# Kernel tuning notes

Hardware: AMD Instinct MI355X
Metric: run time of the kernel (lower is better)

The kernel has to match this reference:

```python
import jax, jax.numpy as jnp
import numpy as np

B, L, D = 4, 2048, 1024
H, DH = 16, 64
W = 128            # window_len
CS, R = 32, 1      # chunk_size, chunk_rank
CACHE = 2048
NCC = CACHE // CS * R   # compressed cache vectors (64)
NCB = L // CS * R       # compressed block vectors (64)
NC = NCC + NCB          # total compressed vectors (128)
NQ = L // CS            # query chunks (64)
T = L // W              # query tiles (16)
NEG = jnp.float32(-1e30)


def _ln(x, g, b, eps=1e-5):
    m = x.mean(-1, keepdims=True)
    v = ((x - m) ** 2).mean(-1, keepdims=True)
    return (x - m) * jax.lax.rsqrt(v + eps) * g + b


def _scores(x, Wd, bd):
    # dconv_1 + per-chunk softmax over chunk_size positions
    b = x.shape[0]; nc = x.shape[1] // CS
    s = (x @ Wd + bd).reshape(b, nc, CS, H, R)
    s = jnp.transpose(s, (0, 3, 1, 4, 2))          # b,H,nc,R,CS
    return jax.nn.softmax(s.astype(jnp.float32), axis=-1).astype(x.dtype)


def _compress(x, sc):
    b = x.shape[0]; nc = x.shape[1] // CS
    xv = jnp.transpose(x.reshape(b, nc, CS, H, DH), (0, 3, 1, 2, 4))  # b,H,nc,CS,DH
    return (sc @ xv).reshape(b, H, nc * R, DH)


def _heads(x):
    b, l, _ = x.shape
    return jnp.transpose(x.reshape(b, l, H, DH), (0, 2, 1, 3))


def _rel_shift(x):
    # Transformer-XL style relative shift, chunk variant (zeros enter from padding)
    b = x.shape[0]; nc = x.shape[-1]
    x5 = jnp.transpose(x.reshape(b, H, NQ, CS, nc), (0, 1, 3, 2, 4))  # b,H,CS,NQ,nc
    xp = jnp.pad(x5, ((0, 0), (0, 0), (0, 0), (0, 0), (0, R))).reshape(b, H, CS, NQ * (nc + R))
    idx = NQ * R + jnp.arange(NQ)[:, None] * nc + jnp.arange(nc)[None, :]
    out = jnp.take(xp, idx.reshape(-1), axis=-1).reshape(b, H, CS, NQ, nc)
    return jnp.transpose(out, (0, 1, 3, 2, 4)).reshape(b, H, L, nc)


def _forward(h, h_cache, key_pe, pos_win, Wq, Wk, Wv, Wo, Wd, bd, Wr, br, Wrc, brc,
             r_r_bias, r_w_bias, g_dproj, b_dproj, g_win, b_win, mask):
    b = h.shape[0]
    q = _heads(h @ Wq) / np.float32(np.sqrt(DH))       # b,H,L,DH (pre-scaled)

    # --- compressed cache keys/values ---
    hcc = _compress(h_cache, _scores(h_cache, Wd, bd))           # b,H,NCC,DH
    hcm = jnp.transpose(hcc, (0, 2, 1, 3)).reshape(b, -1, D)
    k_cache = _heads(_ln(hcm @ Wk, g_dproj, b_dproj))
    v_cache = _heads(_ln(hcm @ Wv, g_dproj, b_dproj))

    # --- sliding window keys/values (last W of cache + current block) ---
    k_bp = h @ Wk
    v_bp = h @ Wv
    hw = h_cache[:, -W:]
    k_win = _ln(jnp.concatenate([hw @ Wk, k_bp], 1), g_win, b_win)   # b, W+L, D
    v_win = _ln(jnp.concatenate([hw @ Wv, v_bp], 1), g_win, b_win)

    # --- compressed current-block keys/values ---
    sc = _scores(h, Wd, bd)
    k_bpc = _heads(_ln(jnp.transpose(_compress(k_bp, sc), (0, 2, 1, 3)).reshape(b, -1, D), g_dproj, b_dproj))
    v_bpc = _heads(_ln(jnp.transpose(_compress(v_bp, sc), (0, 2, 1, 3)).reshape(b, -1, D), g_dproj, b_dproj))
    k_comp = jnp.concatenate([k_cache, k_bpc], 2)     # b,H,NC,DH
    v_comp = jnp.concatenate([v_cache, v_bpc], 2)

    # --- windowed attention (tiled, as_strided equivalent via gather) ---
    ti = jnp.arange(T)[:, None] * W + jnp.arange(2 * W)[None, :]     # (T, 2W)
    k_t = jnp.transpose(k_win[:, ti].reshape(b, T, 2 * W, H, DH), (0, 3, 1, 2, 4))  # b,H,T,2W,DH
    v_t = jnp.transpose(v_win[:, ti].reshape(b, T, 2 * W, H, DH), (0, 3, 1, 2, 4))
    q_t = q.reshape(b, H, T, W, DH)
    aw = jnp.einsum('bhtqd,bhtkd->bhtqk', q_t + r_w_bias, k_t)       # b,H,T,W,2W
    # diagonal extraction: row q keeps cols q+1 .. q+W (the W causal window keys)
    dcol = jnp.arange(W)[:, None] + 1 + jnp.arange(W)[None, :]       # (W, W)
    aw = jnp.take_along_axis(aw, dcol[None, None, None], axis=-1).reshape(b, H, L, W)
    pos_t = (pos_win @ Wr + br).reshape(W, H, DH)
    aw = aw + jnp.einsum('bhld,whd->bhlw', q + r_r_bias, pos_t)

    # --- compressed (chunk) attention ---
    ac = jnp.einsum('bhld,bhcd->bhlc', q, k_comp)
    pos_c = (key_pe @ Wrc + brc).reshape(NC, H, DH)
    ac = ac + _rel_shift(jnp.einsum('bhld,chd->bhlc', q, pos_c))
    ac = jnp.where(mask, NEG, ac.reshape(b, H, NQ, CS, NC)).reshape(b, H, L, NC)

    # --- joint softmax over [compressed | window] ---
    full = jax.nn.softmax(jnp.concatenate([ac, aw], -1).astype(jnp.float32), -1).astype(h.dtype)
    ac, aw = full[..., :NC], full[..., NC:]

    # --- put_tiles: scatter window probs back to tiled 2W layout (inverse of diag extract) ---
    awt = aw.reshape(b, H, T, W, W)
    awp = jnp.pad(awt, ((0, 0), (0, 0), (0, 0), (0, 0), (1, W)))     # last dim 1+2W, zeros outside band
    col = jnp.clip(jnp.arange(2 * W)[None, :] - jnp.arange(W)[:, None], 0, 2 * W)
    aw_t = jnp.take_along_axis(awp, col[None, None, None], axis=-1)  # b,H,T,W,2W

    out = jnp.einsum('bhlc,bhcd->bhld', ac, v_comp) + \
          jnp.einsum('bhtqk,bhtkd->bhtqd', aw_t, v_t).reshape(b, H, L, DH)
    out = jnp.transpose(out, (0, 2, 1, 3)).reshape(b, L, D)
    return out @ Wo


def setup_inputs() -> dict:
    key = jax.random.key(0)
    ks = jax.random.split(key, 16)
    p = lambda i, shape: jax.random.normal(ks[i], shape, jnp.float32) * 0.02
    inp = dict(
        h=jax.random.normal(ks[0], (B, L, D), jnp.float32),
        h_cache=jax.random.normal(ks[1], (B, CACHE, D), jnp.float32),
        key_pe=jax.random.normal(ks[2], (NC, D), jnp.float32),
        pos_embed_window=jax.random.normal(ks[3], (W, D), jnp.float32),
        Wq=p(4, (D, D)), Wk=p(5, (D, D)), Wv=p(6, (D, D)), Wo=p(7, (D, D)),
        Wd=p(8, (D, H * R)), bd=jnp.zeros((H * R,), jnp.float32),
        Wr=p(9, (D, D)), br=jnp.zeros((D,), jnp.float32),
        Wrc=p(10, (D, D)), brc=jnp.zeros((D,), jnp.float32),
        r_r_bias=p(11, (1, H, 1, DH)), r_w_bias=p(12, (1, H, 1, 1, DH)),
        g_dproj=jnp.ones((D,), jnp.float32), b_dproj=jnp.zeros((D,), jnp.float32),
        g_win=jnp.ones((D,), jnp.float32), b_win=jnp.zeros((D,), jnp.float32),
    )
    # causal mask over compressed vectors: bp chunk c visible to query chunk j only if c < j
    jq = jnp.arange(NQ)[:, None]
    cc = jnp.arange(NCB // R)[None, :]
    mbp = jnp.repeat(cc >= jq, R, axis=1)                         # (NQ, NCB)
    mask = jnp.concatenate([jnp.zeros((NQ, NCC), bool), mbp], axis=1)
    inp['chunked_attn_mask'] = mask[None, None, :, None, :]       # (1,1,NQ,1,NC)
    return inp


def reference(h, h_cache, key_pe, pos_embed_window, Wq, Wk, Wv, Wo, Wd, bd, Wr, br,
              Wrc, brc, r_r_bias, r_w_bias, g_dproj, b_dproj, g_win, b_win,
              chunked_attn_mask):
    return _forward(h, h_cache, key_pe, pos_embed_window, Wq, Wk, Wv, Wo, Wd, bd,
                    Wr, br, Wrc, brc, r_r_bias, r_w_bias, g_dproj, b_dproj,
                    g_win, b_win, chunked_attn_mask)
```

## Files before the change

kernel.cpp:

```cpp
#include <hip/hip_runtime.h>


typedef unsigned short u16;
typedef __attribute__((ext_vector_type(8))) short short8;
typedef __attribute__((ext_vector_type(4))) float f32x4;

#define NEGINF -1e30f

__device__ __forceinline__ float bf2f(u16 u) {
    union { unsigned int i; float f; } v; v.i = ((unsigned int)u) << 16; return v.f;
}
__device__ __forceinline__ u16 f2bf(float f) {
    union { float fl; unsigned int i; } v; v.fl = f;
    unsigned int x = v.i;
    return (u16)((x + 0x7fffu + ((x >> 16) & 1u)) >> 16);
}
__device__ __forceinline__ short8 ldg8(const u16* p) { return *(const short8*)p; }

__device__ __forceinline__ void async16(const u16* g, u16* l) {
    __builtin_amdgcn_global_load_lds(
        (const __attribute__((address_space(1))) unsigned int*)g,
        (__attribute__((address_space(3))) unsigned int*)l, 16, 0, 0);
}

__global__ __launch_bounds__(256) void cast_all(
    const float* __restrict__ h, const float* __restrict__ hc,
    const float* __restrict__ pos_w, const float* __restrict__ key_pe,
    const float* __restrict__ Wd,
    u16* __restrict__ hB, u16* __restrict__ hcwB,
    u16* __restrict__ pwB, u16* __restrict__ kpeB, u16* __restrict__ WdB)
{
    const int bx = blockIdx.x, tid = threadIdx.x;
    if (bx < 8192) {
        int i = bx * 256 + tid;
        float4 v = ((const float4*)h)[i];
        u16* o = hB + (long)i * 4;
        o[0] = f2bf(v.x); o[1] = f2bf(v.y); o[2] = f2bf(v.z); o[3] = f2bf(v.w);
    } else if (bx < 8704) {
        int i = (bx - 8192) * 256 + tid;
        int flat = i * 4;
        int b = flat >> 17, r = (flat >> 10) & 127, c = flat & 1023;
        float4 v = *(const float4*)(hc + ((long)b * 2048 + 1920 + r) * 1024 + c);
        u16* o = hcwB + (long)flat;
        o[0] = f2bf(v.x); o[1] = f2bf(v.y); o[2] = f2bf(v.z); o[3] = f2bf(v.w);
    } else if (bx < 8832) {
        int i = (bx - 8704) * 256 + tid;
        float4 v = ((const float4*)pos_w)[i];
        u16* o = pwB + (long)i * 4;
        o[0] = f2bf(v.x); o[1] = f2bf(v.y); o[2] = f2bf(v.z); o[3] = f2bf(v.w);
    } else if (bx < 8960) {
        int i = (bx - 8832) * 256 + tid;
        float4 v = ((const float4*)key_pe)[i];
        u16* o = kpeB + (long)i * 4;
        o[0] = f2bf(v.x); o[1] = f2bf(v.y); o[2] = f2bf(v.z); o[3] = f2bf(v.w);
    } else {
        int e = (bx - 8960) * 256 + tid;
        if (e < 16384) WdB[(e & 15) * 1024 + (e >> 4)] = f2bf(Wd[e]);
    }
}

__global__ __launch_bounds__(256) void cast_transpose6(
    const float* __restrict__ W0, const float* __restrict__ W1,
    const float* __restrict__ W2, const float* __restrict__ W3,
    const float* __restrict__ W4, const float* __restrict__ W5,
    u16* __restrict__ D0, u16* __restrict__ D1, u16* __restrict__ D2,
    u16* __restrict__ D3, u16* __restrict__ D4, u16* __restrict__ D5)
{
    const int z = blockIdx.z;
    const float* W = (z == 0) ? W0 : (z == 1) ? W1 : (z == 2) ? W2
                   : (z == 3) ? W3 : (z == 4) ? W4 : W5;
    u16* WT = (z == 0) ? D0 : (z == 1) ? D1 : (z == 2) ? D2
            : (z == 3) ? D3 : (z == 4) ? D4 : D5;

    __shared__ float t[32][33];
    const int bx = blockIdx.x, by = blockIdx.y;
    const int tx = threadIdx.x & 31, ty = threadIdx.x >> 5;
    #pragma unroll
    for (int p = 0; p < 4; ++p) {
        int k = by * 32 + ty + p * 8;
        t[ty + p * 8][tx] = W[(long)k * 1024 + bx * 32 + tx];
    }
    __syncthreads();
    #pragma unroll
    for (int p = 0; p < 4; ++p) {
        int n = ty + p * 8;
        WT[((long)(bx * 32 + n)) * 1024 + by * 32 + tx] = f2bf(t[tx][n]);
    }
}

__global__ __launch_bounds__(512) void gemm_qkv_big(
    const u16* __restrict__ A, const u16* __restrict__ Bt,
    u16* __restrict__ q_ws, u16* __restrict__ kbp, u16* __restrict__ vbp)
{
    const int tid = threadIdx.x;
    const int bm = blockIdx.x, bn = blockIdx.y;
    const int K = 1024, NT = 32;

    __shared__ __align__(16) u16 smem[65536 / 2];
    u16* const As = smem;
    u16* const Bs = smem + 16384;

    const int lane = tid & 63, wv = tid >> 6;
    const int l15 = lane & 15, quad = lane >> 4;
    const int wm = (wv >> 2) * 128, wn = (wv & 3) * 64;

    f32x4 acc[8][4];
    #pragma unroll
    for (int i = 0; i < 8; ++i)
        #pragma unroll
        for (int j = 0; j < 4; ++j) acc[i][j] = (f32x4){0.f, 0.f, 0.f, 0.f};

    const int r_in = lane >> 2, col8 = (lane & 3) * 8;
    const bool isA = (wv < 4);
    const int crow0 = (isA ? wv : wv - 4) * 64;
    const u16* gb = isA ? (A + (long)(bm * 256 + crow0 + r_in) * K)
                        : (Bt + (long)(bn * 256 + crow0 + r_in) * K);
    const u16* s0 = gb + col8;
    const u16* s1 = s0 + (long)16 * K;
    const u16* s2 = s0 + (long)32 * K;
    const u16* s3 = s0 + (long)48 * K;
    u16* const lb = (isA ? As : Bs) + crow0 * 32;

    auto stage = [&](int buf) {
        u16* d = lb + buf * 8192;
        async16(s0, d);
        async16(s1, d + 512);
        async16(s2, d + 1024);
        async16(s3, d + 1536);
        s0 += 32; s1 += 32; s2 += 32; s3 += 32;
    };

    stage(0);
    for (int t = 0; t < NT; ++t) {
        __builtin_amdgcn_s_barrier();
        if (t + 1 < NT) {
            stage((t + 1) & 1);
            asm volatile("s_waitcnt vmcnt(4) lgkmcnt(0)\ns_barrier" ::: "memory");
        } else {
            asm volatile("s_waitcnt vmcnt(0) lgkmcnt(0)\ns_barrier" ::: "memory");
        }
        const u16* as = As + (t & 1) * 8192;
        const u16* bs = Bs + (t & 1) * 8192;
        short8 af[8], bfr[4];
        #pragma unroll
        for (int i = 0; i < 8; ++i)
            af[i] = *(const short8*)&as[(wm + i * 16 + l15) * 32 + quad * 8];
        #pragma unroll
        for (int j = 0; j < 4; ++j)
            bfr[j] = *(const short8*)&bs[(wn + j * 16 + l15) * 32 + quad * 8];
        #pragma unroll
        for (int i = 0; i < 8; ++i)
            #pragma unroll
            for (int j = 0; j < 4; ++j)
                acc[i][j] = __builtin_amdgcn_mfma_f32_16x16x32_bf16(af[i], bfr[j], acc[i][j], 0, 0, 0);
    }

    const int mat = bn >> 2;
    u16* const outp = (mat == 0) ? q_ws : (mat == 1) ? kbp : vbp;
    const float scl = (mat == 0) ? 0.125f : 1.f;
    const int colbase = (bn & 3) * 256;
    #pragma unroll
    for (int hh = 0; hh < 2; ++hh) {
        __syncthreads();
        if ((wv >> 2) == hh) {
            #pragma unroll
            for (int i = 0; i < 8; ++i) {
                #pragma unroll
                for (int j = 0; j < 4; ++j) {
                    const int row = i * 16 + quad * 4;
                    const int col = wn + j * 16 + l15;
                    smem[(row + 0) * 256 + col] = f2bf(acc[i][j][0] * scl);
                    smem[(row + 1) * 256 + col] = f2bf(acc[i][j][1] * scl);
                    smem[(row + 2) * 256 + col] = f2bf(acc[i][j][2] * scl);
                    smem[(row + 3) * 256 + col] = f2bf(acc[i][j][3] * scl);
                }
            }
        }
        __syncthreads();
        #pragma unroll
        for (int k = 0; k < 8; ++k) {
            const int seg = tid + k * 512;
            const int row = seg >> 5, c16 = seg & 31;
            short8 v = *(const short8*)&smem[row * 256 + c16 * 8];
            *(short8*)(outp + (long)(bm * 256 + hh * 128 + row) * 1024 + colbase + c16 * 8) = v;
        }
    }
}

#define GEMM_P3_BODY(EPILOGUE)                                                  \
    const int tid = threadIdx.x;                                                \
    const int bm = blockIdx.x, bn = blockIdx.y;                                 \
    const int K = 1024, NT = 32;                                                \
    __shared__ __align__(16) u16 As[3 * 128 * 32];                              \
    __shared__ __align__(16) u16 Bs[3 * 128 * 32];                              \
    const int lane = tid & 63, wv = tid >> 6;                                   \
    const int l15 = lane & 15, quad = lane >> 4;                                \
    const int wm = (wv & 1) * 64, wn = (wv >> 1) * 64;                          \
    f32x4 acc[4][4];                                                            \
    _Pragma("unroll")                                                           \
    for (int i = 0; i < 4; ++i)                                                 \
        _Pragma("unroll")                                                       \
        for (int j = 0; j < 4; ++j) acc[i][j] = (f32x4){0.f, 0.f, 0.f, 0.f};    \
    const int srow = wv * 32 + (lane >> 2);                                     \
    const int scol = (lane & 3) * 8;                                            \
    const u16* a_src  = A  + (long)(bm * 128 + srow) * K + scol;                \
    const u16* a_src2 = a_src + (long)16 * K;                                   \
    const u16* b_src  = Bt + (long)(bn * 128 + srow) * K + scol;                \
    const u16* b_src2 = b_src + (long)16 * K;                                   \
    const int lofs0 = (wv * 32) * 32;                                           \
    const int lofs1 = (wv * 32 + 16) * 32;                                      \
    auto stage = [&](int t, int cur) {                                          \
        const int k0 = t * 32;                                                  \
        async16(a_src  + k0, &As[cur * 4096 + lofs0]);                          \
        async16(a_src2 + k0, &As[cur * 4096 + lofs1]);                          \
        async16(b_src  + k0, &Bs[cur * 4096 + lofs0]);                          \
        async16(b_src2 + k0, &Bs[cur * 4096 + lofs1]);                          \
    };                                                                          \
    stage(0, 0); stage(1, 1);                                                   \
    int cur = 0;                                                                \
    for (int t = 0; t < NT; ++t) {                                              \
        if (t == NT - 1)                                                        \
            asm volatile("s_waitcnt vmcnt(0) lgkmcnt(0)\ns_barrier" ::: "memory"); \
        else                                                                    \
            asm volatile("s_waitcnt vmcnt(4) lgkmcnt(0)\ns_barrier" ::: "memory"); \
        int nxt = cur + 2; if (nxt >= 3) nxt -= 3;                              \
        if (t + 2 < NT) stage(t + 2, nxt);                                      \
        const u16* as = &As[cur * 4096];                                        \
        const u16* bs = &Bs[cur * 4096];                                        \
        short8 af[4], bfr[4];                                                   \
        _Pragma("unroll")                                                       \
        for (int i = 0; i < 4; ++i)                                             \
            af[i] = *(const short8*)&as[(wm + i * 16 + l15) * 32 + quad * 8];   \
        _Pragma("unroll")                                                       \
        for (int j = 0; j < 4; ++j)                                             \
            bfr[j] = *(const short8*)&bs[(wn + j * 16 + l15) * 32 + quad * 8];  \
        _Pragma("unroll")                                                       \
        for (int i = 0; i < 4; ++i)                                             \
            _Pragma("unroll")                                                   \
            for (int j = 0; j < 4; ++j)                                         \
                acc[i][j] = __builtin_amdgcn_mfma_f32_16x16x32_bf16(af[i], bfr[j], acc[i][j], 0, 0, 0); \
        cur = (cur + 1 == 3) ? 0 : cur + 1;                                     \
    }                                                                           \
    EPILOGUE

__global__ __launch_bounds__(256) void gemm_out3(
    const u16* __restrict__ A, const u16* __restrict__ Bt,
    float* __restrict__ Cf)
{
    GEMM_P3_BODY({
        _Pragma("unroll")
        for (int i = 0; i < 4; ++i) {
            _Pragma("unroll")
            for (int j = 0; j < 4; ++j) {
                int col = bn * 128 + wn + j * 16 + l15;
                _Pragma("unroll")
                for (int r = 0; r < 4; ++r) {
                    int row = bm * 128 + wm + i * 16 + quad * 4 + r;
                    Cf[(long)row * 1024 + col] = acc[i][j][r];
                }
            }
        }
    })
}

struct GJob {
    const u16* A; long ab;
    const u16* Bt;
    float* Cf; u16* Cb; long cb;
    const float* bias; float scale;
};

__device__ __forceinline__ void gemm_core128(
    const GJob& j, int bz, int bm, int bn, int N, int K)
{
    const int tid = threadIdx.x;
    const u16* A = j.A + (long)bz * j.ab;
    const long coff = (long)bz * j.cb;

    __shared__ __align__(16) u16 As[128 * 32];
    __shared__ __align__(16) u16 Bs[128 * 32];

    const int lane = tid & 63, wv = tid >> 6;
    const int l15 = lane & 15, quad = lane >> 4;
    const int wm = (wv & 1) * 64, wn = (wv >> 1) * 64;

    f32x4 acc[4][4];
    #pragma unroll
    for (int i = 0; i < 4; ++i)
        #pragma unroll
        for (int jx = 0; jx < 4; ++jx) acc[i][jx] = (f32x4){0.f, 0.f, 0.f, 0.f};

    const int srow = wv * 32 + (lane >> 2);
    const int scol = (lane & 3) * 8;
    const u16* a_src  = A    + (long)(bm * 128 + srow) * K + scol;
    const u16* a_src2 = a_src + (long)16 * K;
    const u16* b_src  = j.Bt + (long)(bn * 128 + srow) * K + scol;
    const u16* b_src2 = b_src + (long)16 * K;
    u16* lA0 = &As[(wv * 32) * 32];
    u16* lA1 = &As[(wv * 32 + 16) * 32];
    u16* lB0 = &Bs[(wv * 32) * 32];
    u16* lB1 = &Bs[(wv * 32 + 16) * 32];

    for (int k0 = 0; k0 < K; k0 += 32) {
        async16(a_src, lA0); async16(a_src2, lA1);
        async16(b_src, lB0); async16(b_src2, lB1);
        a_src += 32; a_src2 += 32; b_src += 32; b_src2 += 32;
        __syncthreads();
        short8 af[4], bfr[4];
        #pragma unroll
        for (int i = 0; i < 4; ++i)
            af[i] = *(const short8*)&As[(wm + i * 16 + l15) * 32 + quad * 8];
        #pragma unroll
        for (int jx = 0; jx < 4; ++jx)
            bfr[jx] = *(const short8*)&Bs[(wn + jx * 16 + l15) * 32 + quad * 8];
        #pragma unroll
        for (int i = 0; i < 4; ++i)
            #pragma unroll
            for (int jx = 0; jx < 4; ++jx)
                acc[i][jx] = __builtin_amdgcn_mfma_f32_16x16x32_bf16(af[i], bfr[jx], acc[i][jx], 0, 0, 0);
        __syncthreads();
    }

    #pragma unroll
    for (int i = 0; i < 4; ++i) {
        #pragma unroll
        for (int jx = 0; jx < 4; ++jx) {
            int col = bn * 128 + wn + jx * 16 + l15;
            float bsv = j.bias ? j.bias[col] : 0.f;
            #pragma unroll
            for (int r = 0; r < 4; ++r) {
                int row = bm * 128 + wm + i * 16 + quad * 4 + r;
                float v = acc[i][jx][r] * j.scale + bsv;
                long idx = coff + (long)row * N + col;
                if (j.Cf) j.Cf[idx] = v;
                if (j.Cb) j.Cb[idx] = f2bf(v);
            }
        }
    }
}

__global__ __launch_bounds__(256) void gemm_dual(GJob j0, GJob j1, int nz0, int N, int K)
{
    const bool first = ((int)blockIdx.z < nz0);
    const int bz = first ? blockIdx.z : blockIdx.z - nz0;
    if (first) gemm_core128(j0, bz, blockIdx.x, blockIdx.y, N, K);
    else       gemm_core128(j1, bz, blockIdx.x, blockIdx.y, N, K);
}

__global__ __launch_bounds__(256) void gemm_multi4(GJob j0, GJob j1, GJob j2, GJob j3,
                                                   int n0, int n1, int n2, int N, int K)
{
    const int z = blockIdx.z;
    if (z < n0)                gemm_core128(j0, z, blockIdx.x, blockIdx.y, N, K);
    else if (z < n0 + n1)      gemm_core128(j1, z - n0, blockIdx.x, blockIdx.y, N, K);
    else if (z < n0 + n1 + n2) gemm_core128(j2, z - n0 - n1, blockIdx.x, blockIdx.y, N, K);
    else                       gemm_core128(j3, z - n0 - n1 - n2, blockIdx.x, blockIdx.y, N, K);
}

__global__ __launch_bounds__(256) void scores_compress2(
    const float* __restrict__ hc, const u16* __restrict__ hBp,
    const u16* __restrict__ WdB, const float* __restrict__ bd,
    u16* __restrict__ hcm, float* __restrict__ sc_blk)
{
    const int c = blockIdx.x, b = blockIdx.y;
    const bool zc = (blockIdx.z == 0);
    const int tid = threadIdx.x;
    const int lane = tid & 63, wv = tid >> 6;
    const int l15 = lane & 15, quad = lane >> 4;

    __shared__ __align__(16) u16 srcs[32][1032];
    __shared__ float sred[4][32][16];
    __shared__ float s_sm[32][16];

    if (zc) {
        const float* sb = hc + (long)b * 2048 * 1024 + (long)c * 32 * 1024;
        for (int e = tid; e < 8192; e += 256) {
            int flat = e * 4;
            int row = flat >> 10, col = flat & 1023;
            float4 v = *(const float4*)(sb + (long)row * 1024 + col);
            u16* dp = &srcs[row][col];
            dp[0] = f2bf(v.x); dp[1] = f2bf(v.y); dp[2] = f2bf(v.z); dp[3] = f2bf(v.w);
        }
    } else {
        const u16* sb = hBp + (long)b * 2048 * 1024 + (long)c * 32 * 1024;
        for (int e = tid; e < 4096; e += 256) {
            int flat = e * 8;
            int row = flat >> 10, col = flat & 1023;
            *(short8*)&srcs[row][col] = ldg8(sb + (long)row * 1024 + col);
        }
    }
    __syncthreads();

    {
        f32x4 acc0 = {0.f,0.f,0.f,0.f}, acc1 = {0.f,0.f,0.f,0.f};
        const int kq = wv * 256;
        #pragma unroll
        for (int kc = 0; kc < 8; ++kc) {
            int off = kq + kc * 32 + quad * 8;
            short8 bf_ = ldg8(WdB + (long)l15 * 1024 + off);
            short8 a0 = *(const short8*)&srcs[l15][off];
            short8 a1 = *(const short8*)&srcs[16 + l15][off];
            acc0 = __builtin_amdgcn_mfma_f32_16x16x32_bf16(a0, bf_, acc0, 0, 0, 0);
            acc1 = __builtin_amdgcn_mfma_f32_16x16x32_bf16(a1, bf_, acc1, 0, 0, 0);
        }
        #pragma unroll
        for (int r = 0; r < 4; ++r) {
            sred[wv][quad * 4 + r][l15]      = acc0[r];
            sred[wv][16 + quad * 4 + r][l15] = acc1[r];
        }
    }
    __syncthreads();
    for (int idx = tid; idx < 512; idx += 256) {
        int i = idx >> 4, hd = idx & 15;
        s_sm[i][hd] = bd[hd] + sred[0][i][hd] + sred[1][i][hd]
                            + sred[2][i][hd] + sred[3][i][hd];
    }
    __syncthreads();

    if (tid < 16) {
        int hd = tid;
        float m = NEGINF;
        for (int i = 0; i < 32; ++i) m = fmaxf(m, s_sm[i][hd]);
        float s = 0.f;
        for (int i = 0; i < 32; ++i) s += __expf(s_sm[i][hd] - m);
        float inv = 1.f / s;
        for (int i = 0; i < 32; ++i) s_sm[i][hd] = __expf(s_sm[i][hd] - m) * inv;
    }
    __syncthreads();

    if (!zc) {
        for (int idx = tid; idx < 512; idx += 256) {
            int hd = idx >> 5, i = idx & 31;
            sc_blk[(long)b * (16*64*32) + ((long)hd * 64 + c) * 32 + i] = s_sm[i][hd];
        }
    } else {
        #pragma unroll
        for (int p = 0; p < 4; ++p) {
            int j = tid + p * 256;
            int hd = j >> 6;
            float acc = 0.f;
            for (int i = 0; i < 32; ++i) acc += s_sm[i][hd] * bf2f(srcs[i][j]);
            hcm[(long)b * (64*1024) + (long)c * 1024 + j] = f2bf(acc);
        }
    }
}

__global__ __launch_bounds__(256) void compress_kv_ln(
    const u16* __restrict__ kbp, const u16* __restrict__ vbp,
    const float* __restrict__ sc,
    const float* __restrict__ g, const float* __restrict__ be,
    u16* __restrict__ k_comp, u16* __restrict__ vcT)
{
    const int c = blockIdx.x, b = blockIdx.y;
    const int tid = threadIdx.x;
    const int lane = tid & 63, wv = tid >> 6;

    __shared__ float scw[16][32];
    __shared__ float red[4][4];

    for (int idx = tid; idx < 512; idx += 256) {
        int hd = idx >> 5, i = idx & 31;
        scw[hd][i] = sc[((long)(b * 16 + hd) * 64 + c) * 32 + i];
    }
    __syncthreads();

    const int j0 = tid * 4;
    const int hd = j0 >> 6;
    float xk[4] = {0.f,0.f,0.f,0.f}, xv[4] = {0.f,0.f,0.f,0.f};
    const u16* kb = kbp + ((long)b * 2048 + c * 32) * 1024 + j0;
    const u16* vb = vbp + ((long)b * 2048 + c * 32) * 1024 + j0;
    for (int i = 0; i < 32; ++i) {
        float w = scw[hd][i];
        uint2 kr = *(const uint2*)(kb + (long)i * 1024);
        uint2 vr = *(const uint2*)(vb + (long)i * 1024);
        const u16* kp = (const u16*)&kr;
        const u16* vp = (const u16*)&vr;
        #pragma unroll
        for (int p = 0; p < 4; ++p) {
            xk[p] += w * bf2f(kp[p]);
            xv[p] += w * bf2f(vp[p]);
        }
    }
    float sk = 0.f, qk = 0.f, sv = 0.f, qv = 0.f;
    #pragma unroll
    for (int p = 0; p < 4; ++p) { sk += xk[p]; qk += xk[p]*xk[p]; sv += xv[p]; qv += xv[p]*xv[p]; }
    for (int off = 32; off; off >>= 1) {
        sk += __shfl_xor(sk, off); qk += __shfl_xor(qk, off);
        sv += __shfl_xor(sv, off); qv += __shfl_xor(qv, off);
    }
    if (lane == 0) { red[0][wv] = sk; red[1][wv] = qk; red[2][wv] = sv; red[3][wv] = qv; }
    __syncthreads();
    sk = red[0][0] + red[0][1] + red[0][2] + red[0][3];
    qk = red[1][0] + red[1][1] + red[1][2] + red[1][3];
    sv = red[2][0] + red[2][1] + red[2][2] + red[2][3];
    qv = red[3][0] + red[3][1] + red[3][2] + red[3][3];
    const float inv_n = 1.f / 1024.f;
    float mk = sk * inv_n, mv = sv * inv_n;
    float ik = rsqrtf(fmaxf(qk * inv_n - mk * mk, 0.f) + 1e-5f);
    float iv = rsqrtf(fmaxf(qv * inv_n - mv * mv, 0.f) + 1e-5f);
    float4 g4 = *(const float4*)(g + j0);
    float4 b4 = *(const float4*)(be + j0);
    float gg[4] = {g4.x, g4.y, g4.z, g4.w};
    float bb[4] = {b4.x, b4.y, b4.z, b4.w};
    u16 ko[4];
    #pragma unroll
    for (int p = 0; p < 4; ++p) ko[p] = f2bf((xk[p] - mk) * ik * gg[p] + bb[p]);
    *(uint2*)&k_comp[((long)b * 128 + 64 + c) * 1024 + j0] = *(const uint2*)ko;
    #pragma unroll
    for (int p = 0; p < 4; ++p)
        vcT[((long)b * 1024 + j0 + p) * 128 + 64 + c] = f2bf((xv[p] - mv) * iv * gg[p] + bb[p]);
}

__global__ __launch_bounds__(256) void ln_rows_kv(
    const float* __restrict__ kc, const float* __restrict__ vc,
    const float* __restrict__ g, const float* __restrict__ be,
    u16* __restrict__ k_comp, u16* __restrict__ vcT)
{
    const int gr = blockIdx.x;
    const int b = gr >> 6, r = gr & 63;
    const float* pk = kc + ((long)b * 64 + r) * 1024;
    const float* pv = vc + ((long)b * 64 + r) * 1024;
    const int tid = threadIdx.x;
    const int lane = tid & 63, wv = tid >> 6;

    __shared__ float red[4][4];
    float xk[4], xv[4];
    float smk = 0.f, sqk = 0.f, smv = 0.f, sqv = 0.f;
    #pragma unroll
    for (int p = 0; p < 4; ++p) {
        xk[p] = pk[tid + p * 256];
        xv[p] = pv[tid + p * 256];
        smk += xk[p]; sqk += xk[p] * xk[p];
        smv += xv[p]; sqv += xv[p] * xv[p];
    }
    for (int off = 32; off; off >>= 1) {
        smk += __shfl_xor(smk, off); sqk += __shfl_xor(sqk, off);
        smv += __shfl_xor(smv, off); sqv += __shfl_xor(sqv, off);
    }
    if (lane == 0) { red[0][wv] = smk; red[1][wv] = sqk; red[2][wv] = smv; red[3][wv] = sqv; }
    __syncthreads();
    smk = red[0][0] + red[0][1] + red[0][2] + red[0][3];
    sqk = red[1][0] + red[1][1] + red[1][2] + red[1][3];
    smv = red[2][0] + red[2][1] + red[2][2] + red[2][3];
    sqv = red[3][0] + red[3][1] + red[3][2] + red[3][3];
    const float inv_n = 1.f / 1024.f;
    float mk = smk * inv_n, mv = smv * inv_n;
    float ik = rsqrtf(fmaxf(sqk * inv_n - mk * mk, 0.f) + 1e-5f);
    float iv = rsqrtf(fmaxf(sqv * inv_n - mv * mv, 0.f) + 1e-5f);
    #pragma unroll
    for (int p = 0; p < 4; ++p) {
        int j = tid + p * 256;
        k_comp[((long)b * 128 + r) * 1024 + j] = f2bf((xk[p] - mk) * ik * g[j] + be[j]);
        vcT[((long)b * 1024 + j) * 128 + r]    = f2bf((xv[p] - mv) * iv * g[j] + be[j]);
    }
}

__global__ __launch_bounds__(256) void row_stats_all(
    const float* __restrict__ kcw, const float* __restrict__ vcw,
    const u16* __restrict__ kbp, const u16* __restrict__ vbp,
    float2* __restrict__ st_k, float2* __restrict__ st_v)
{
    const int gr = blockIdx.x;
    const int tid = threadIdx.x;
    const int lane = tid & 63, wv = tid >> 6;

    float sm1 = 0.f, sq1 = 0.f, sm2 = 0.f, sq2 = 0.f;
    long dst;
    if (gr < 512) {
        const int b = gr >> 7, r = gr & 127;
        const float* p1 = kcw + ((long)b * 128 + r) * 1024;
        const float* p2 = vcw + ((long)b * 128 + r) * 1024;
        #pragma unroll
        for (int p = 0; p < 4; ++p) {
            float x = p1[tid + p * 256];
            float y = p2[tid + p * 256];
            sm1 += x; sq1 += x * x;
            sm2 += y; sq2 += y * y;
        }
        dst = (long)b * 2176 + r;
    } else {
        const int g2 = gr - 512;
        const int b = g2 >> 11, r = g2 & 2047;
        const u16* p1 = kbp + ((long)b * 2048 + r) * 1024 + tid * 4;
        const u16* p2 = vbp + ((long)b * 2048 + r) * 1024 + tid * 4;
        uint2 v1 = *(const uint2*)p1;
        uint2 v2 = *(const uint2*)p2;
        const u16* a1 = (const u16*)&v1;
        const u16* a2 = (const u16*)&v2;
        #pragma unroll
        for (int p = 0; p < 4; ++p) {
            float x = bf2f(a1[p]);
            float y = bf2f(a2[p]);
            sm1 += x; sq1 += x * x;
            sm2 += y; sq2 += y * y;
        }
        dst = (long)b * 2176 + 128 + r;
    }

    __shared__ float red[4][4];
    for (int off = 32; off; off >>= 1) {
        sm1 += __shfl_xor(sm1, off); sq1 += __shfl_xor(sq1, off);
        sm2 += __shfl_xor(sm2, off); sq2 += __shfl_xor(sq2, off);
    }
    if (lane == 0) { red[0][wv] = sm1; red[1][wv] = sq1; red[2][wv] = sm2; red[3][wv] = sq2; }
    __syncthreads();
    if (tid == 0) {
        sm1 = red[0][0] + red[0][1] + red[0][2] + red[0][3];
        sq1 = red[1][0] + red[1][1] + red[1][2] + red[1][3];
        sm2 = red[2][0] + red[2][1] + red[2][2] + red[2][3];
        sq2 = red[3][0] + red[3][1] + red[3][2] + red[3][3];
        float m1 = sm1 * (1.f / 1024.f);
        float i1 = rsqrtf(fmaxf(sq1 * (1.f / 1024.f) - m1 * m1, 0.f) + 1e-5f);
        float m2 = sm2 * (1.f / 1024.f);
        float i2 = rsqrtf(fmaxf(sq2 * (1.f / 1024.f) - m2 * m2, 0.f) + 1e-5f);
        st_k[dst] = make_float2(m1, i1);
        st_v[dst] = make_float2(m2, i2);
    }
}

__global__ __launch_bounds__(256) void win_apply(
    const float* __restrict__ kcw, const float* __restrict__ vcw,
    const u16* __restrict__ kbp, const u16* __restrict__ vbp,
    const float2* __restrict__ st_kw, const float2* __restrict__ st_vw,
    const float* __restrict__ g_w, const float* __restrict__ b_w,
    u16* __restrict__ kwin, u16* __restrict__ vwinT)
{
    const int tt = blockIdx.x, dc = blockIdx.y, b = blockIdx.z;
    const int t0 = tt * 64, d0 = dc * 64;
    const int tid = threadIdx.x;

    __shared__ u16 vt[64][74];

    const int r = tid >> 2;
    const int dsub = (tid & 3) * 16;
    const int t = t0 + r;
    float2 sk = st_kw[(long)b * 2176 + t];
    float2 sv = st_vw[(long)b * 2176 + t];
    const float* ksf = kcw + ((long)b * 128 + t) * 1024;
    const float* vsf = vcw + ((long)b * 128 + t) * 1024;
    const u16*   ksb = kbp + ((long)b * 2048 + t - 128) * 1024;
    const u16*   vsb = vbp + ((long)b * 2048 + t - 128) * 1024;
    #pragma unroll
    for (int j = 0; j < 16; j += 4) {
        int d = d0 + dsub + j;
        float4 kv, vv;
        if (t < 128) {
            kv = *(const float4*)(ksf + d);
            vv = *(const float4*)(vsf + d);
        } else {
            uint2 kr = *(const uint2*)(ksb + d);
            uint2 vr = *(const uint2*)(vsb + d);
            const u16* kp = (const u16*)&kr;
            const u16* vp = (const u16*)&vr;
            kv = make_float4(bf2f(kp[0]), bf2f(kp[1]), bf2f(kp[2]), bf2f(kp[3]));
            vv = make_float4(bf2f(vp[0]), bf2f(vp[1]), bf2f(vp[2]), bf2f(vp[3]));
        }
        float4 g4 = *(const float4*)(g_w + d);
        float4 b4 = *(const float4*)(b_w + d);
        u16 ko[4];
        ko[0] = f2bf((kv.x - sk.x) * sk.y * g4.x + b4.x);
        ko[1] = f2bf((kv.y - sk.x) * sk.y * g4.y + b4.y);
        ko[2] = f2bf((kv.z - sk.x) * sk.y * g4.z + b4.z);
        ko[3] = f2bf((kv.w - sk.x) * sk.y * g4.w + b4.w);
        *(uint2*)&kwin[((long)b * 2176 + t) * 1024 + d] = *(const uint2*)ko;
        vt[r][dsub + j + 0] = f2bf((vv.x - sv.x) * sv.y * g4.x + b4.x);
        vt[r][dsub + j + 1] = f2bf((vv.y - sv.x) * sv.y * g4.y + b4.y);
        vt[r][dsub + j + 2] = f2bf((vv.z - sv.x) * sv.y * g4.z + b4.z);
        vt[r][dsub + j + 3] = f2bf((vv.w - sv.x) * sv.y * g4.w + b4.w);
    }
    __syncthreads();
    #pragma unroll
    for (int pass = 0; pass < 16; ++pass) {
        int dd = (tid >> 6) + pass * 4;
        int rr = tid & 63;
        int crow = t0 + rr;
        if (crow >= 1)
            vwinT[((long)b * 1024 + d0 + dd) * 2176 + crow - 1] = vt[rr][dd];
    }
}

__global__ __launch_bounds__(256, 4) void attention(
    const u16* __restrict__ qb,
    const u16* __restrict__ kcb,
    const u16* __restrict__ vcT,
    const u16* __restrict__ kwb,
    const u16* __restrict__ vwT,
    const u16* __restrict__ pcb,
    const u16* __restrict__ ptb,
    const float* __restrict__ r_w,
    const float* __restrict__ r_r,
    u16* __restrict__ attn_o)
{
    const int qc = blockIdx.x, h = blockIdx.y, b = blockIdx.z;
    const int l0 = qc * 32;
    const int tid = threadIdx.x;
    const int lane = tid & 63, wv = tid >> 6;
    const int l15 = lane & 15, quad = lane >> 4;

    __shared__ __align__(16) float L[32 * 260];
    __shared__ __align__(16) u16 qa[32][72];
    u16* Lu = (u16*)L;

    {
        const int r = tid >> 3, d0 = (tid & 7) * 8;
        short8 qv = ldg8(qb + ((long)(b * 2048 + l0 + r)) * 1024 + h * 64 + d0);
        *(short8*)&qa[r][d0] = qv;
    }
    __syncthreads();

    __builtin_amdgcn_s_setprio(1);
    #pragma unroll
    for (int ti = 0; ti < 2; ++ti) {
        int n0 = (wv * 2 + ti) * 16;
        int ci = n0 + l15;
        f32x4 a0 = {0.f,0.f,0.f,0.f}, a1 = {0.f,0.f,0.f,0.f};
        if (n0 < 64 + qc) {
            int p = 64 + ci - qc; if (p > 127) p = 127;
            #pragma unroll
            for (int kc = 0; kc < 2; ++kc) {
                int k0 = kc * 32;
                short8 bk = ldg8(kcb + ((long)(b * 128 + ci)) * 1024 + h * 64 + k0 + quad * 8);
                short8 bp = ldg8(pcb + (long)p * 1024 + h * 64 + k0 + quad * 8);
                short8 fa0 = *(const short8*)&qa[l15][k0 + quad * 8];
                short8 fa1 = *(const short8*)&qa[16 + l15][k0 + quad * 8];
                a0 = __builtin_amdgcn_mfma_f32_16x16x32_bf16(fa0, bk, a0, 0, 0, 0);
                a0 = __builtin_amdgcn_mfma_f32_16x16x32_bf16(fa0, bp, a0, 0, 0, 0);
                a1 = __builtin_amdgcn_mfma_f32_16x16x32_bf16(fa1, bk, a1, 0, 0, 0);
                a1 = __builtin_amdgcn_mfma_f32_16x16x32_bf16(fa1, bp, a1, 0, 0, 0);
            }
        }
        bool msk = (ci >= 64 + qc);
        #pragma unroll
        for (int r = 0; r < 4; ++r) {
            L[(quad * 4 + r) * 260 + ci]      = msk ? NEGINF : a0[r];
            L[(16 + quad * 4 + r) * 260 + ci] = msk ? NEGINF : a1[r];
        }
    }

    {
        short8 qf[2][2];
        #pragma unroll
        for (int kc = 0; kc < 2; ++kc) {
            const int off = kc * 32 + quad * 8;
            const float* bp_ = r_r + h * 64 + off;
            float4 b0 = *(const float4*)bp_;
            float4 b1 = *(const float4*)(bp_ + 4);
            float bb[8] = {b0.x,b0.y,b0.z,b0.w,b1.x,b1.y,b1.z,b1.w};
            #pragma unroll
            for (int hf = 0; hf < 2; ++hf) {
                short8 qv = *(const short8*)&qa[hf * 16 + l15][off];
                short8 f;
                #pragma unroll
                for (int j = 0; j < 8; ++j) f[j] = (short)f2bf(bf2f((u16)qv[j]) + bb[j]);
                qf[kc][hf] = f;
            }
        }
        #pragma unroll
        for (int ti = 0; ti < 2; ++ti) {
            int w0 = (wv * 2 + ti) * 16;
            int w = w0 + l15;
            f32x4 a0 = {0.f,0.f,0.f,0.f}, a1 = {0.f,0.f,0.f,0.f};
            #pragma unroll
            for (int kc = 0; kc < 2; ++kc) {
                int k0 = kc * 32;
                short8 bp = ldg8(ptb + (long)w * 1024 + h * 64 + k0 + quad * 8);
                a0 = __builtin_amdgcn_mfma_f32_16x16x32_bf16(qf[kc][0], bp, a0, 0, 0, 0);
                a1 = __builtin_amdgcn_mfma_f32_16x16x32_bf16(qf[kc][1], bp, a1, 0, 0, 0);
            }
            #pragma unroll
            for (int r = 0; r < 4; ++r) {
                L[(quad * 4 + r) * 260 + 128 + w]      = a0[r];
                L[(16 + quad * 4 + r) * 260 + 128 + w] = a1[r];
            }
        }
    }

    f32x4 s1a[3], s1b[3];
    int nts[3]; int nw = 0;
    {
        short8 qf[2][2];
        #pragma unroll
        for (int kc = 0; kc < 2; ++kc) {
            const int off = kc * 32 + quad * 8;
            const float* bp_ = r_w + h * 64 + off;
            float4 b0 = *(const float4*)bp_;
            float4 b1 = *(const float4*)(bp_ + 4);
            float bb[8] = {b0.x,b0.y,b0.z,b0.w,b1.x,b1.y,b1.z,b1.w};
            #pragma unroll
            for (int hf = 0; hf < 2; ++hf) {
                short8 qv = *(const short8*)&qa[hf * 16 + l15][off];
                short8 f;
                #pragma unroll
                for (int j = 0; j < 8; ++j) f[j] = (short)f2bf(bf2f((u16)qv[j]) + bb[j]);
                qf[kc][hf] = f;
            }
        }
        for (int nt = wv; nt < 10; nt += 4) {
            int t = nt * 16 + l15;
            int row = l0 + 1 + t; if (row > 2175) row = 2175;
            f32x4 a0 = {0.f,0.f,0.f,0.f}, a1 = {0.f,0.f,0.f,0.f};
            #pragma unroll
            for (int kc = 0; kc < 2; ++kc) {
                int k0 = kc * 32;
                short8 bk = ldg8(kwb + ((long)(b * 2176 + row)) * 1024 + h * 64 + k0 + quad * 8);
                a0 = __builtin_amdgcn_mfma_f32_16x16x32_bf16(qf[kc][0], bk, a0, 0, 0, 0);
                a1 = __builtin_amdgcn_mfma_f32_16x16x32_bf16(qf[kc][1], bk, a1, 0, 0, 0);
            }
            s1a[nw] = a0; s1b[nw] = a1; nts[nw] = nt; ++nw;
        }
    }
    __builtin_amdgcn_s_setprio(0);
    __syncthreads();
    for (int i = 0; i < nw; ++i) {
        int t = nts[i] * 16 + l15;
        #pragma unroll
        for (int r = 0; r < 4; ++r) {
            int r0 = quad * 4 + r;
            int w0 = t - r0;
            if (w0 >= 0 && w0 < 128) L[r0 * 260 + 128 + w0] += s1a[i][r];
            int r1 = 16 + quad * 4 + r;
            int w1 = t - r1;
            if (w1 >= 0 && w1 < 128) L[r1 * 260 + 128 + w1] += s1b[i][r];
        }
    }
    __syncthreads();

    const int n0d = wv * 16;
    short8 bvv[9];
    {
        const u16* vc = vcT + ((long)(b * 1024 + h * 64 + n0d + l15)) * 128 + quad * 8;
        #pragma unroll
        for (int kc = 0; kc < 4; ++kc) bvv[kc] = ldg8(vc + kc * 32);
        const u16* vw = vwT + ((long)(b * 1024 + h * 64 + n0d + l15)) * 2176 + l0 + quad * 8;
        #pragma unroll
        for (int kc = 0; kc < 5; ++kc) bvv[4 + kc] = ldg8(vw + kc * 32);
    }

    #pragma unroll
    for (int rr = 0; rr < 8; ++rr) {
        const int r = wv * 8 + rr;
        float4 v = *(const float4*)&L[r * 260 + lane * 4];
        float m = fmaxf(fmaxf(v.x, v.y), fmaxf(v.z, v.w));
        for (int off = 32; off; off >>= 1) m = fmaxf(m, __shfl_xor(m, off));
        float e0 = __expf(v.x - m), e1 = __expf(v.y - m);
        float e2 = __expf(v.z - m), e3 = __expf(v.w - m);
        float s = (e0 + e1) + (e2 + e3);
        for (int off = 32; off; off >>= 1) s += __shfl_xor(s, off);
        float inv = 1.f / s;
        e0 *= inv; e1 *= inv; e2 *= inv; e3 *= inv;
        u16* rowP = Lu + (long)r * 520;
        if (lane < 32) {
            u16 pk[4] = {f2bf(e0), f2bf(e1), f2bf(e2), f2bf(e3)};
            *(uint2*)&rowP[lane * 4] = *(const uint2*)pk;
        } else {
            const int l = lane - 32;
            const int t = 4 * l + r;
            u16* p = rowP + 160 + t;
            p[0] = f2bf(e0); p[1] = f2bf(e1); p[2] = f2bf(e2); p[3] = f2bf(e3);
            const int tz = (l < r) ? l : 128 + l;
            rowP[160 + tz] = 0;
        }
    }
    __syncthreads();

    __builtin_amdgcn_s_setprio(1);
    f32x4 o0 = {0.f,0.f,0.f,0.f}, o1 = {0.f,0.f,0.f,0.f};
    #pragma unroll
    for (int kc = 0; kc < 4; ++kc) {
        int k0 = kc * 32;
        short8 av0 = *(const short8*)(Lu + (long)l15 * 520 + k0 + quad * 8);
        short8 av1 = *(const short8*)(Lu + (long)(16 + l15) * 520 + k0 + quad * 8);
        o0 = __builtin_amdgcn_mfma_f32_16x16x32_bf16(av0, bvv[kc], o0, 0, 0, 0);
        o1 = __builtin_amdgcn_mfma_f32_16x16x32_bf16(av1, bvv[kc], o1, 0, 0, 0);
    }
    #pragma unroll
    for (int kc = 0; kc < 5; ++kc) {
        int k0 = kc * 32;
        short8 av0 = *(const short8*)(Lu + (long)l15 * 520 + 160 + k0 + quad * 8);
        short8 av1 = *(const short8*)(Lu + (long)(16 + l15) * 520 + 160 + k0 + quad * 8);
        o0 = __builtin_amdgcn_mfma_f32_16x16x32_bf16(av0, bvv[4 + kc], o0, 0, 0, 0);
        o1 = __builtin_amdgcn_mfma_f32_16x16x32_bf16(av1, bvv[4 + kc], o1, 0, 0, 0);
    }
    __builtin_amdgcn_s_setprio(0);
    #pragma unroll
    for (int r = 0; r < 4; ++r) {
        int r0 = quad * 4 + r, r1 = 16 + quad * 4 + r;
        attn_o[((long)(b * 2048 + l0 + r0)) * 1024 + h * 64 + n0d + l15] = f2bf(o0[r]);
        attn_o[((long)(b * 2048 + l0 + r1)) * 1024 + h * 64 + n0d + l15] = f2bf(o1[r]);
    }
}

extern "C" void kernel_launch(void* const* d_in, const int* in_sizes, int n_in,
                              void* d_out, int out_size, void* d_ws, size_t ws_size,
                              hipStream_t stream)
{
    (void)in_sizes; (void)n_in; (void)out_size; (void)ws_size;

    const float* h       = (const float*)d_in[0];
    const float* h_cache = (const float*)d_in[1];
    const float* key_pe  = (const float*)d_in[2];
    const float* pos_w   = (const float*)d_in[3];
    const float* Wq      = (const float*)d_in[4];
    const float* Wk      = (const float*)d_in[5];
    const float* Wv      = (const float*)d_in[6];
    const float* Wo      = (const float*)d_in[7];
    const float* Wd      = (const float*)d_in[8];
    const float* bd      = (const float*)d_in[9];
    const float* Wr      = (const float*)d_in[10];
    const float* br      = (const float*)d_in[11];
    const float* Wrc     = (const float*)d_in[12];
    const float* brc     = (const float*)d_in[13];
    const float* r_r     = (const float*)d_in[14];
    const float* r_w     = (const float*)d_in[15];
    const float* g_d     = (const float*)d_in[16];
    const float* b_d     = (const float*)d_in[17];
    const float* g_w     = (const float*)d_in[18];
    const float* b_w     = (const float*)d_in[19];

    char* ws = (char*)d_ws;
    size_t off = 0;
    auto alloc = [&](size_t bytes) -> void* {
        void* p = ws + off; off += (bytes + 255) & ~(size_t)255; return p;
    };
    u16* hB     = (u16*)alloc((size_t)8192 * 1024 * 2);
    u16* hcwB   = (u16*)alloc((size_t)4 * 128 * 1024 * 2);
    u16* WqkvT  = (u16*)alloc((size_t)3 * 1024 * 1024 * 2);
    u16* WoT    = (u16*)alloc((size_t)1024 * 1024 * 2);
    u16* WrT    = (u16*)alloc((size_t)1024 * 1024 * 2);
    u16* WrcT   = (u16*)alloc((size_t)1024 * 1024 * 2);
    u16* pwB    = (u16*)alloc((size_t)128 * 1024 * 2);
    u16* kpeB   = (u16*)alloc((size_t)128 * 1024 * 2);
    u16* WdB    = (u16*)alloc((size_t)16 * 1024 * 2);
    u16*   q_ws   = (u16*)alloc((size_t)8192 * 1024 * 2);
    u16*   kbp    = (u16*)alloc((size_t)8192 * 1024 * 2);
    u16*   vbp    = (u16*)alloc((size_t)8192 * 1024 * 2);
    u16*   attn_o = (u16*)alloc((size_t)8192 * 1024 * 2);
    float* kcw    = (float*)alloc((size_t)4 * 128 * 1024 * 4);
    float* vcw    = (float*)alloc((size_t)4 * 128 * 1024 * 4);
    u16*   hcm    = (u16*)alloc((size_t)4 * 64 * 1024 * 2);
    float* kc_raw = (float*)alloc((size_t)4 * 64 * 1024 * 4);
    float* vc_raw = (float*)alloc((size_t)4 * 64 * 1024 * 4);
    float* sc_blk = (float*)alloc((size_t)4 * 16 * 64 * 32 * 4);
    u16*   k_comp = (u16*)alloc((size_t)4 * 128 * 1024 * 2);
    u16*   vcT    = (u16*)alloc((size_t)4 * 1024 * 128 * 2);
    float2* st_kw = (float2*)alloc((size_t)4 * 2176 * 8);
    float2* st_vw = (float2*)alloc((size_t)4 * 2176 * 8);
    u16*   pos_tb = (u16*)alloc((size_t)128 * 1024 * 2);
    u16*   pos_cb = (u16*)alloc((size_t)128 * 1024 * 2);
    u16*   kwin   = (u16*)alloc((size_t)4 * 2176 * 1024 * 2);
    u16*   vwinT  = (u16*)alloc((size_t)4 * 1024 * 2176 * 2 + 256);

    const u16* WkT = WqkvT + (size_t)1024 * 1024;
    const u16* WvT = WqkvT + (size_t)2 * 1024 * 1024;

    const dim3 blk(256);

    cast_all<<<dim3(9024), blk, 0, stream>>>(h, h_cache, pos_w, key_pe, Wd,
                                             hB, hcwB, pwB, kpeB, WdB);
    cast_transpose6<<<dim3(32,32,6), blk, 0, stream>>>(
        Wq, Wk, Wv, Wo, Wr, Wrc,
        WqkvT, WqkvT + (size_t)1024*1024, WqkvT + (size_t)2*1024*1024,
        WoT, WrT, WrcT);

    {
        GJob jk = { hcwB, (long)128*1024, WkT, kcw, nullptr, (long)128*1024, nullptr, 1.f };
        GJob jv = { hcwB, (long)128*1024, WvT, vcw, nullptr, (long)128*1024, nullptr, 1.f };
        GJob jt = { pwB,  0, WrT,  nullptr, pos_tb, 0, br,  1.f };
        GJob jc = { kpeB, 0, WrcT, nullptr, pos_cb, 0, brc, 1.f };
        gemm_multi4<<<dim3(1,8,10), blk, 0, stream>>>(jk, jv, jt, jc, 4, 4, 1, 1024, 1024);
    }

    gemm_qkv_big<<<dim3(32,12), dim3(512), 0, stream>>>(hB, WqkvT, q_ws, kbp, vbp);

    scores_compress2<<<dim3(64,4,2), blk, 0, stream>>>(h_cache, hB, WdB, bd, hcm, sc_blk);

    {
        GJob jk = { hcm, 0, WkT, kc_raw, nullptr, 0, nullptr, 1.f };
        GJob jv = { hcm, 0, WvT, vc_raw, nullptr, 0, nullptr, 1.f };
        gemm_dual<<<dim3(2,8,2), blk, 0, stream>>>(jk, jv, 1, 1024, 1024);
    }

    compress_kv_ln<<<dim3(64,4), blk, 0, stream>>>(kbp, vbp, sc_blk, g_d, b_d, k_comp, vcT);
    ln_rows_kv<<<dim3(256), blk, 0, stream>>>(kc_raw, vc_raw, g_d, b_d, k_comp, vcT);

    row_stats_all<<<dim3(8704), blk, 0, stream>>>(kcw, vcw, kbp, vbp, st_kw, st_vw);
    win_apply<<<dim3(34,16,4), blk, 0, stream>>>(kcw, vcw, kbp, vbp, st_kw, st_vw, g_w, b_w, kwin, vwinT);

    attention<<<dim3(64,16,4), blk, 0, stream>>>(q_ws, k_comp, vcT, kwin, vwinT,
                                                 pos_cb, pos_tb, r_w, r_r, attn_o);
    gemm_out3<<<dim3(64,8,1), blk, 0, stream>>>(attn_o, WoT, (float*)d_out);
}
```

Measured before the change: 467.3 us.

## Swizzle GEMM LDS tiles and merge compressed-cache KV GEMMs into multi-job launch

Applies an XOR swizzle to the 16-byte column chunks in the LDS tiles of the big QKV GEMM and the pipelined GEMM body, on both the async global-to-LDS writes and the fragment reads. This is meant to reduce LDS bank conflicts when loading MFMA operands. Separately, scores_compress2 is moved ahead so that the compressed-cache K/V projections can join the window/positional GEMMs in a single six-job launch, removing one kernel launch and increasing concurrency. The cost is some blocks that exit immediately because of the per-job row-block bound.

```diff
diff --git a/kernel.cpp b/kernel.cpp
--- a/kernel.cpp
+++ b/kernel.cpp
@@ -110,7 +110,8 @@
         #pragma unroll
         for (int j = 0; j < 4; ++j) acc[i][j] = (f32x4){0.f, 0.f, 0.f, 0.f};
 
-    const int r_in = lane >> 2, col8 = (lane & 3) * 8;
+    const int r_in = lane >> 2;
+    const int col8 = (((lane & 3) ^ ((lane >> 3) & 3)) * 8);
     const bool isA = (wv < 4);
     const int crow0 = (isA ? wv : wv - 4) * 64;
     const u16* gb = isA ? (A + (long)(bm * 256 + crow0 + r_in) * K)
@@ -130,6 +131,8 @@
         s0 += 32; s1 += 32; s2 += 32; s3 += 32;
     };
 
+    const int ssl = (quad ^ ((l15 >> 1) & 3)) * 8;
+
     stage(0);
     for (int t = 0; t < NT; ++t) {
         __builtin_amdgcn_s_barrier();
@@ -144,10 +147,10 @@
         short8 af[8], bfr[4];
         #pragma unroll
         for (int i = 0; i < 8; ++i)
-            af[i] = *(const short8*)&as[(wm + i * 16 + l15) * 32 + quad * 8];
+            af[i] = *(const short8*)&as[(wm + i * 16 + l15) * 32 + ssl];
         #pragma unroll
         for (int j = 0; j < 4; ++j)
-            bfr[j] = *(const short8*)&bs[(wn + j * 16 + l15) * 32 + quad * 8];
+            bfr[j] = *(const short8*)&bs[(wn + j * 16 + l15) * 32 + ssl];
         #pragma unroll
         for (int i = 0; i < 8; ++i)
             #pragma unroll
@@ -202,7 +205,7 @@
         _Pragma("unroll")                                                       \
         for (int j = 0; j < 4; ++j) acc[i][j] = (f32x4){0.f, 0.f, 0.f, 0.f};    \
     const int srow = wv * 32 + (lane >> 2);                                     \
-    const int scol = (lane & 3) * 8;                                            \
+    const int scol = (((lane & 3) ^ ((lane >> 3) & 3)) * 8);                    \
     const u16* a_src  = A  + (long)(bm * 128 + srow) * K + scol;                \
     const u16* a_src2 = a_src + (long)16 * K;                                   \
     const u16* b_src  = Bt + (long)(bn * 128 + srow) * K + scol;                \
@@ -217,6 +220,7 @@
         async16(b_src2 + k0, &Bs[cur * 4096 + lofs1]);                          \
     };                                                                          \
     stage(0, 0); stage(1, 1);                                                   \
+    const int ssl = (quad ^ ((l15 >> 1) & 3)) * 8;                              \
     int cur = 0;                                                                \
     for (int t = 0; t < NT; ++t) {                                              \
         if (t == NT - 1)                                                        \
@@ -230,10 +234,10 @@
         short8 af[4], bfr[4];                                                   \
         _Pragma("unroll")                                                       \
         for (int i = 0; i < 4; ++i)                                             \
-            af[i] = *(const short8*)&as[(wm + i * 16 + l15) * 32 + quad * 8];   \
+            af[i] = *(const short8*)&as[(wm + i * 16 + l15) * 32 + ssl];        \
         _Pragma("unroll")                                                       \
         for (int j = 0; j < 4; ++j)                                             \
-            bfr[j] = *(const short8*)&bs[(wn + j * 16 + l15) * 32 + quad * 8];  \
+            bfr[j] = *(const short8*)&bs[(wn + j * 16 + l15) * 32 + ssl];       \
         _Pragma("unroll")                                                       \
         for (int i = 0; i < 4; ++i)                                             \
             _Pragma("unroll")                                                   \
@@ -268,6 +272,7 @@
     const u16* Bt;
     float* Cf; u16* Cb; long cb;
     const float* bias; float scale;
+    int bmN;
 };
 
 __device__ __forceinline__ void gemm_core128(
@@ -339,22 +344,20 @@
     }
 }
 
-__global__ __launch_bounds__(256) void gemm_dual(GJob j0, GJob j1, int nz0, int N, int K)
-{
-    const bool first = ((int)blockIdx.z < nz0);
-    const int bz = first ? blockIdx.z : blockIdx.z - nz0;
-    if (first) gemm_core128(j0, bz, blockIdx.x, blockIdx.y, N, K);
-    else       gemm_core128(j1, bz, blockIdx.x, blockIdx.y, N, K);
-}
-
-__global__ __launch_bounds__(256) void gemm_multi4(GJob j0, GJob j1, GJob j2, GJob j3,
-                                                   int n0, int n1, int n2, int N, int K)
+__global__ __launch_bounds__(256) void gemm_multi6(
+    GJob j0, GJob j1, GJob j2, GJob j3, GJob j4, GJob j5,
+    int n0, int n1, int n2, int n3, int n4, int N, int K)
 {
     const int z = blockIdx.z;
-    if (z < n0)                gemm_core128(j0, z, blockIdx.x, blockIdx.y, N, K);
-    else if (z < n0 + n1)      gemm_core128(j1, z - n0, blockIdx.x, blockIdx.y, N, K);
-    else if (z < n0 + n1 + n2) gemm_core128(j2, z - n0 - n1, blockIdx.x, blockIdx.y, N, K);
-    else                       gemm_core128(j3, z - n0 - n1 - n2, blockIdx.x, blockIdx.y, N, K);
+    GJob j; int bz;
+    if (z < n0)                          { j = j0; bz = z; }
+    else if (z < n0 + n1)                { j = j1; bz = z - n0; }
+    else if (z < n0 + n1 + n2)           { j = j2; bz = z - n0 - n1; }
+    else if (z < n0 + n1 + n2 + n3)      { j = j3; bz = z - n0 - n1 - n2; }
+    else if (z < n0 + n1 + n2 + n3 + n4) { j = j4; bz = z - n0 - n1 - n2 - n3; }
+    else                                 { j = j5; bz = z - n0 - n1 - n2 - n3 - n4; }
+    if ((int)blockIdx.x >= j.bmN) return;
+    gemm_core128(j, bz, blockIdx.x, blockIdx.y, N, K);
 }
 
 __global__ __launch_bounds__(256) void scores_compress2(
@@ -962,23 +965,20 @@
         WqkvT, WqkvT + (size_t)1024*1024, WqkvT + (size_t)2*1024*1024,
         WoT, WrT, WrcT);
 
+    scores_compress2<<<dim3(64,4,2), blk, 0, stream>>>(h_cache, hB, WdB, bd, hcm, sc_blk);
+
     {
-        GJob jk = { hcwB, (long)128*1024, WkT, kcw, nullptr, (long)128*1024, nullptr, 1.f };
-        GJob jv = { hcwB, (long)128*1024, WvT, vcw, nullptr, (long)128*1024, nullptr, 1.f };
-        GJob jt = { pwB,  0, WrT,  nullptr, pos_tb, 0, br,  1.f };
-        GJob jc = { kpeB, 0, WrcT, nullptr, pos_cb, 0, brc, 1.f };
-        gemm_multi4<<<dim3(1,8,10), blk, 0, stream>>>(jk, jv, jt, jc, 4, 4, 1, 1024, 1024);
+        GJob jk  = { hcwB, (long)128*1024, WkT, kcw, nullptr, (long)128*1024, nullptr, 1.f, 1 };
+        GJob jv  = { hcwB, (long)128*1024, WvT, vcw, nullptr, (long)128*1024, nullptr, 1.f, 1 };
+        GJob jt  = { pwB,  0, WrT,  nullptr, pos_tb, 0, br,  1.f, 1 };
+        GJob jc  = { kpeB, 0, WrcT, nullptr, pos_cb, 0, brc, 1.f, 1 };
+        GJob jkc = { hcm, 0, WkT, kc_raw, nullptr, 0, nullptr, 1.f, 2 };
+        GJob jvc = { hcm, 0, WvT, vc_raw, nullptr, 0, nullptr, 1.f, 2 };
+        gemm_multi6<<<dim3(2,8,12), blk, 0, stream>>>(jk, jv, jt, jc, jkc, jvc,
+                                                      4, 4, 1, 1, 1, 1024, 1024);
     }
 
     gemm_qkv_big<<<dim3(32,12), dim3(512), 0, stream>>>(hB, WqkvT, q_ws, kbp, vbp);
-
-    scores_compress2<<<dim3(64,4,2), blk, 0, stream>>>(h_cache, hB, WdB, bd, hcm, sc_blk);
-
-    {
-        GJob jk = { hcm, 0, WkT, kc_raw, nullptr, 0, nullptr, 1.f };
-        GJob jv = { hcm, 0, WvT, vc_raw, nullptr, 0, nullptr, 1.f };
-        gemm_dual<<<dim3(2,8,2), blk, 0, stream>>>(jk, jv, 1, 1024, 1024);
-    }
 
     compress_kv_ln<<<dim3(64,4), blk, 0, stream>>>(kbp, vbp, sc_blk, g_d, b_d, k_comp, vcT);
     ln_rows_kv<<<dim3(256), blk, 0, stream>>>(kc_raw, vc_raw, g_d, b_d, k_comp, vcT);
```

Measured after the change: 436.5 us. 6.6% less time.
